# Kernel optimization log

Hardware: AMD Instinct MI355X
Metric: run time of the kernel (lower is better)

The kernel has to match this reference:

```python
import jax, jax.numpy as jnp
import numpy as np

NUM_HEADS = 8
REGION_SIZE = 16
TOPK = 8


def setup_inputs() -> dict:
    key = jax.random.key(0)
    ks = jax.random.split(key, 3)
    B, T, C = 4, 2048, 512
    x = jax.random.normal(ks[0], (B, T, C), dtype=jnp.float32)
    # nn.Linear weights stored as (in, out) so y = x @ W + b
    Wqkv = jax.random.normal(ks[1], (C, 3 * C), dtype=jnp.float32) * 0.02
    bqkv = jnp.zeros((3 * C,), dtype=jnp.float32)
    Wout = jax.random.normal(ks[2], (C, C), dtype=jnp.float32) * 0.02
    bout = jnp.zeros((C,), dtype=jnp.float32)
    return {"x": x, "Wqkv": Wqkv, "bqkv": bqkv, "Wout": Wout, "bout": bout}


def reference(x, Wqkv, bqkv, Wout, bout):
    B, T, C = x.shape
    H, R, K = NUM_HEADS, REGION_SIZE, TOPK
    Dh = C // H
    Nr = T // R  # T chosen divisible by R, so no padding branch
    scale = 1.0 / (Dh ** 0.5)

    qkv = x @ Wqkv + bqkv                                  # (B,T,3C)
    qkv = qkv.reshape(B, T, 3, H, Dh).transpose(2, 0, 3, 1, 4)  # (3,B,H,T,Dh)
    q = qkv[0].reshape(B, H, Nr, R, Dh)
    k = qkv[1].reshape(B, H, Nr, R, Dh)
    v = qkv[2].reshape(B, H, Nr, R, Dh)

    # region-average scores and top-k region selection
    q_avg = q.mean(axis=3)                                 # (B,H,Nr,Dh)
    k_avg = k.mean(axis=3)
    region_score = jnp.einsum('bhqd,bhkd->bhqk', q_avg, k_avg) * scale
    _, topk_idx = jax.lax.top_k(region_score, K)           # (B,H,Nr,K)

    # gather selected K/V region blocks (no dense expand)
    bi = jnp.arange(B)[:, None, None, None]
    hi = jnp.arange(H)[None, :, None, None]
    k_sel = k[bi, hi, topk_idx]                            # (B,H,Nr,K,R,Dh)
    v_sel = v[bi, hi, topk_idx]                            # (B,H,Nr,K,R,Dh)

    # block-sparse attention: each query attends to its K selected regions
    logits = jnp.einsum('bhnrd,bhnksd->bhnrks', q, k_sel) * scale
    logits = logits.reshape(B, H, Nr, R, K * R)
    attn = jax.nn.softmax(logits, axis=-1)
    out = jnp.einsum('bhnrk,bhnkd->bhnrd', attn, v_sel.reshape(B, H, Nr, K * R, Dh))

    out = out.reshape(B, H, T, Dh).transpose(0, 2, 1, 3).reshape(B, T, C)
    return out @ Wout + bout
```

## Files before the change

kernel.cpp:

```cpp
#include <hip/hip_runtime.h>
#include <hip/hip_bf16.h>
#include <math.h>

typedef __bf16 bf16x8 __attribute__((ext_vector_type(8)));
typedef float f32x4 __attribute__((ext_vector_type(4)));

namespace {
constexpr int B  = 4;
constexpr int T  = 2048;
constexpr int C  = 512;
constexpr int H  = 8;
constexpr int Dh = 64;
constexpr int R  = 16;
constexpr int Nr = 128;
constexpr int K  = 8;
constexpr int BT = B * T;
constexpr int QKV_N = 3 * C;
constexpr int KD = 512;
constexpr float SCALE = 0.125f;
}

static __device__ __forceinline__ unsigned short f2bf(float f) {
  unsigned int u = __float_as_uint(f);
  u += 0x7fffu + ((u >> 16) & 1u);
  return (unsigned short)(u >> 16);
}

static __device__ __forceinline__ unsigned cvt_pk_bf16(float lo, float hi) {
  unsigned r;
  asm("v_cvt_pk_bf16_f32 %0, %1, %2" : "=v"(r) : "v"(lo), "v"(hi));
  return r;
}

static __device__ __forceinline__ void gload16(const unsigned short* g, unsigned short* l) {
  __builtin_amdgcn_global_load_lds(
      (const __attribute__((address_space(1))) unsigned int*)g,
      (__attribute__((address_space(3))) unsigned int*)l, 16, 0, 0);
}

static __device__ __forceinline__ unsigned fkey(float f) {
  unsigned u = __float_as_uint(f);
  return (u & 0x80000000u) ? ~u : (u ^ 0x80000000u);
}

__global__ __launch_bounds__(256) void convert_x_kernel(
    const float4* __restrict__ x, ushort4* __restrict__ xbf) {
  const int i = blockIdx.x * 256 + threadIdx.x;
  const float4 v = x[i];
  ushort4 o;
  o.x = f2bf(v.x); o.y = f2bf(v.y); o.z = f2bf(v.z); o.w = f2bf(v.w);
  xbf[i] = o;
}

__global__ __launch_bounds__(256) void transpose_convert_kernel(
    const float* __restrict__ W, unsigned short* __restrict__ Wt, int Kd, int Nd) {
  __shared__ float tile[32][33];
  const int n0 = blockIdx.x * 32, k0 = blockIdx.y * 32;
  const int tx = threadIdx.x & 31, ty = threadIdx.x >> 5;
#pragma unroll
  for (int i = 0; i < 32; i += 8)
    tile[ty + i][tx] = W[(size_t)(k0 + ty + i) * Nd + (n0 + tx)];
  __syncthreads();
#pragma unroll
  for (int i = 0; i < 32; i += 8)
    Wt[(size_t)(n0 + ty + i) * Kd + (k0 + tx)] = f2bf(tile[tx][ty + i]);
}

__device__ __forceinline__ void mfma_mainloop(
    const unsigned short* __restrict__ A, const unsigned short* __restrict__ Bt,
    int bm, int bn, unsigned short* As, unsigned short* Bs, f32x4 (&acc)[4][4]) {
  const int tid = threadIdx.x;
  const int wave = tid >> 6, lane = tid & 63;
  const int wr = wave >> 1, wc = wave & 1;
  const unsigned short* ga = A  + (size_t)(bm + wave * 16 + (lane >> 2)) * KD + (lane & 3) * 8;
  const unsigned short* gb = Bt + (size_t)(bn + wave * 16 + (lane >> 2)) * KD + (lane & 3) * 8;
  unsigned short* lA = As + wave * 512;
  unsigned short* lB = Bs + wave * 512;
  const int fr = lane & 15, kg = lane >> 4;
  const unsigned short* rA = As + (wr * 64 + fr) * 32 + kg * 8;
  const unsigned short* rB = Bs + (wc * 64 + fr) * 32 + kg * 8;
  for (int k0 = 0; k0 < KD; k0 += 32) {
    gload16(ga + k0,                    lA);
    gload16(ga + (size_t)64 * KD + k0,  lA + 2048);
    gload16(gb + k0,                    lB);
    gload16(gb + (size_t)64 * KD + k0,  lB + 2048);
    __syncthreads();
    bf16x8 a[4], b[4];
#pragma unroll
    for (int m = 0; m < 4; ++m) a[m] = *(const bf16x8*)(rA + m * 512);
#pragma unroll
    for (int n = 0; n < 4; ++n) b[n] = *(const bf16x8*)(rB + n * 512);
#pragma unroll
    for (int m = 0; m < 4; ++m)
#pragma unroll
      for (int n = 0; n < 4; ++n)
        acc[m][n] = __builtin_amdgcn_mfma_f32_16x16x32_bf16(a[m], b[n], acc[m][n], 0, 0, 0);
    __syncthreads();
  }
}

__global__ __launch_bounds__(256) void qkv_gemm_mfma_kernel(
    const unsigned short* __restrict__ xbf, const unsigned short* __restrict__ Wt,
    const float* __restrict__ bias,
    unsigned short* __restrict__ qbf, unsigned short* __restrict__ kbf,
    unsigned short* __restrict__ vt) {
  __shared__ unsigned short As[128 * 32];
  __shared__ unsigned short Bs[128 * 32];
  f32x4 acc[4][4] = {};
  const int id = (blockIdx.x & 7) * 96 + (blockIdx.x >> 3);
  const int bn = (id % 12) * 128, bm = (id / 12) * 128;
  mfma_mainloop(xbf, Wt, bm, bn, As, Bs, acc);
  const int lane = threadIdx.x & 63, wave = threadIdx.x >> 6;
  const int wr = wave >> 1, wc = wave & 1;
  const int scol = bn + wc * 64;
  const int s = scol >> 9, h = (scol >> 6) & 7;
  const int b = bm >> 11, t0b = (bm & (T - 1)) + wr * 64;
  const int bh = b * H + h;
  if (s == 2) {
#pragma unroll
    for (int n = 0; n < 4; ++n) {
      const int d = (n * 16 + (lane & 15));
      const float bv = bias[scol + n * 16 + (lane & 15)];
#pragma unroll
      for (int m = 0; m < 4; ++m) {
        const int t = t0b + m * 16 + (lane >> 4) * 4;
        ushort4 pk;
        pk.x = f2bf(acc[m][n][0] + bv); pk.y = f2bf(acc[m][n][1] + bv);
        pk.z = f2bf(acc[m][n][2] + bv); pk.w = f2bf(acc[m][n][3] + bv);
        *(ushort4*)&vt[((size_t)bh * Dh + d) * T + t] = pk;
      }
    }
  } else {
    unsigned short* dstbase = ((s == 0) ? qbf : kbf) + (size_t)bh * T * Dh;
    const int g = lane >> 4, i = lane & 3, a = (lane >> 2) & 3;
#pragma unroll
    for (int n = 0; n < 4; ++n) {
      const float bv = bias[scol + n * 16 + (lane & 15)];
#pragma unroll
      for (int m = 0; m < 4; ++m) {
        const float v0 = acc[m][n][0] + bv, v1 = acc[m][n][1] + bv;
        const float v2 = acc[m][n][2] + bv, v3 = acc[m][n][3] + bv;
        const unsigned p01 = cvt_pk_bf16(v0, v1);
        const unsigned p23 = cvt_pk_bf16(v2, v3);
        const unsigned u01 = (unsigned)__shfl_xor((int)p01, 1);
        const unsigned u23 = (unsigned)__shfl_xor((int)p23, 1);
        const unsigned A  = (lane & 1) ? ((u01 >> 16) | (p01 & 0xFFFF0000u))
                                       : ((p01 & 0xFFFFu) | (u01 << 16));
        const unsigned Bb = (lane & 1) ? ((u23 >> 16) | (p23 & 0xFFFF0000u))
                                       : ((p23 & 0xFFFFu) | (u23 << 16));
        const unsigned w  = (unsigned)__shfl_xor((int)A, 2);
        const unsigned xw = (unsigned)__shfl_xor((int)Bb, 2);
        uint2 res;
        res.x = (lane & 2) ? xw : A;
        res.y = (lane & 2) ? Bb : w;
        const int t = t0b + m * 16 + 4 * g + i;
        const int d = n * 16 + 4 * a;
        *(uint2*)&dstbase[(size_t)t * Dh + d] = res;
      }
    }
  }
}

__global__ __launch_bounds__(256) void out_gemm_mfma_kernel(
    const unsigned short* __restrict__ Abf, const unsigned short* __restrict__ Wt,
    const float* __restrict__ bias, float* __restrict__ out) {
  __shared__ unsigned short As[128 * 32];
  __shared__ unsigned short Bs[128 * 32];
  f32x4 acc[4][4] = {};
  const int id = (blockIdx.x & 7) * 32 + (blockIdx.x >> 3);
  const int bn = (id & 3) * 128, bm = (id >> 2) * 128;
  mfma_mainloop(Abf, Wt, bm, bn, As, Bs, acc);
  const int lane = threadIdx.x & 63, wave = threadIdx.x >> 6;
  const int wr = wave >> 1, wc = wave & 1;
#pragma unroll
  for (int n = 0; n < 4; ++n) {
    const int col = bn + wc * 64 + n * 16 + (lane & 15);
    const float bv = bias[col];
#pragma unroll
    for (int m = 0; m < 4; ++m) {
      const int row = bm + wr * 64 + m * 16 + (lane >> 4) * 4;
#pragma unroll
      for (int r = 0; r < 4; ++r)
        out[(size_t)(row + r) * C + col] = acc[m][n][r] + bv;
    }
  }
}

__global__ __launch_bounds__(256) void x_avg_kernel(
    const float* __restrict__ x, float* __restrict__ xavg) {
  const int blk = blockIdx.x;
  const int c = threadIdx.x;
  const float* xp = x + (size_t)blk * R * C;
  float s0 = 0.f, s1 = 0.f;
#pragma unroll
  for (int r = 0; r < R; ++r) { s0 += xp[r * C + c]; s1 += xp[r * C + c + 256]; }
  xavg[(size_t)blk * C + c] = s0 * 0.0625f;
  xavg[(size_t)blk * C + c + 256] = s1 * 0.0625f;
}

__global__ __launch_bounds__(512) void qkavg_gemm_kernel(
    const float* __restrict__ Xa, const float* __restrict__ W,
    const float* __restrict__ bias,
    float* __restrict__ qavg, float* __restrict__ kavg) {
  __shared__ float As[32][68];
  __shared__ float Bs[32][68];
  const int tid = threadIdx.x;
  const int bm = blockIdx.y * 64;
  const int bn = blockIdx.x * 64;
  const int tm = (tid >> 5) << 2;
  const int tn = (tid & 31) << 1;
  const int arow = tid >> 3;
  const int acol = (tid & 7) << 2;
  const int brow = tid >> 4;
  const int bcol = (tid & 15) << 2;
  float acc[4][2] = {};
  for (int k0 = 0; k0 < KD; k0 += 32) {
    {
      const float4 a = *(const float4*)&Xa[(size_t)(bm + arow) * KD + (k0 + acol)];
      As[acol + 0][arow] = a.x;
      As[acol + 1][arow] = a.y;
      As[acol + 2][arow] = a.z;
      As[acol + 3][arow] = a.w;
      *(float4*)&Bs[brow][bcol] =
          *(const float4*)&W[(size_t)(k0 + brow) * QKV_N + (bn + bcol)];
    }
    __syncthreads();
#pragma unroll
    for (int kk = 0; kk < 32; ++kk) {
      const float4 av = *(const float4*)&As[kk][tm];
      const float2 bv = *(const float2*)&Bs[kk][tn];
      const float aa[4] = {av.x, av.y, av.z, av.w};
#pragma unroll
      for (int i = 0; i < 4; ++i) {
        acc[i][0] += aa[i] * bv.x;
        acc[i][1] += aa[i] * bv.y;
      }
    }
    __syncthreads();
  }
#pragma unroll
  for (int i = 0; i < 4; ++i) {
    const int m = bm + tm + i;
    const int b = m >> 7, n = m & (Nr - 1);
#pragma unroll
    for (int j = 0; j < 2; ++j) {
      const int col = bn + tn + j;
      const int half = col >> 9, h = (col >> 6) & 7, d = col & 63;
      float* dst = half ? kavg : qavg;
      dst[(((size_t)b * H + h) * Nr + n) * Dh + d] = acc[i][j] + bias[col];
    }
  }
}

__global__ __launch_bounds__(64) void topk_kernel(
    const float* __restrict__ qavg, const float* __restrict__ kavg,
    int* __restrict__ topk) {
  const int blk = blockIdx.x;
  const int bh  = blk >> 7;
  const int lane = threadIdx.x;
  const float qv = qavg[(size_t)blk * Dh + lane];
  const float4* k0p = (const float4*)(kavg + ((size_t)bh * Nr + lane) * Dh);
  const float4* k1p = (const float4*)(kavg + ((size_t)bh * Nr + lane + 64) * Dh);
  float d0 = 0.f, d1 = 0.f;
#pragma unroll
  for (int j = 0; j < 16; ++j) {
    const float4 a = k0p[j];
    const float4 bq = k1p[j];
    const float q0 = __shfl(qv, 4 * j + 0);
    const float q1 = __shfl(qv, 4 * j + 1);
    const float q2 = __shfl(qv, 4 * j + 2);
    const float q3 = __shfl(qv, 4 * j + 3);
    d0 += q0 * a.x;  d0 += q1 * a.y;  d0 += q2 * a.z;  d0 += q3 * a.w;
    d1 += q0 * bq.x; d1 += q1 * bq.y; d1 += q2 * bq.z; d1 += q3 * bq.w;
  }
  float v0 = d0, v1 = d1;
#pragma unroll
  for (int j = 0; j < K; ++j) {
    const unsigned long long c0 =
        ((unsigned long long)fkey(v0) << 32) | (unsigned)(127 - lane);
    const unsigned long long c1 =
        ((unsigned long long)fkey(v1) << 32) | (unsigned)(63 - lane);
    unsigned long long c = (c0 > c1) ? c0 : c1;
#pragma unroll
    for (int off = 1; off < 64; off <<= 1) {
      const unsigned long long o = __shfl_xor(c, off);
      c = (o > c) ? o : c;
    }
    const int idx = 127 - (int)(c & 0xffffffffu);
    if (lane == j) topk[blk * K + j] = idx;
    if (idx == lane) v0 = -INFINITY;
    if (idx == lane + 64) v1 = -INFINITY;
  }
}

__global__ __launch_bounds__(64) void attn_mfma_kernel(
    const unsigned short* __restrict__ qbf, const unsigned short* __restrict__ kbf,
    const unsigned short* __restrict__ vt, const int* __restrict__ topk,
    unsigned short* __restrict__ aoutbf) {
  const int phys = blockIdx.x;
  const int blk = (phys & 7) * 512 + (phys >> 3);
  const int bh = blk >> 7, n = blk & (Nr - 1);
  const int b = bh >> 3, h = bh & 7;
  const int lane = threadIdx.x;
  const int q = lane & 15, kg = lane >> 4;
  const int kg1 = kg & 1, kgh = kg >> 1;

  const int rv = topk[blk * K + (lane & 7)];
  int ridx[8];
#pragma unroll
  for (int j = 0; j < 8; ++j) ridx[j] = __shfl(rv, j);

  const unsigned short* qp = qbf + ((size_t)bh * T + n * R + q) * Dh + kg * 8;
  const bf16x8 qf0 = *(const bf16x8*)(qp);
  const bf16x8 qf1 = *(const bf16x8*)(qp + 32);

  f32x4 s[8];
#pragma unroll
  for (int j = 0; j < 8; ++j) {
    const unsigned short* kp = kbf + ((size_t)bh * T + ridx[j] * R + q) * Dh + kg * 8;
    const bf16x8 kf0 = *(const bf16x8*)(kp);
    const bf16x8 kf1 = *(const bf16x8*)(kp + 32);
    f32x4 acc = {};
    acc = __builtin_amdgcn_mfma_f32_16x16x32_bf16(kf0, qf0, acc, 0, 0, 0);
    acc = __builtin_amdgcn_mfma_f32_16x16x32_bf16(kf1, qf1, acc, 0, 0, 0);
    s[j] = acc;
  }

  float mx = s[0][0];
#pragma unroll
  for (int j = 0; j < 8; ++j)
#pragma unroll
    for (int r = 0; r < 4; ++r) mx = fmaxf(mx, s[j][r]);
  mx = fmaxf(mx, __shfl_xor(mx, 16));
  mx = fmaxf(mx, __shfl_xor(mx, 32));
  float sum = 0.f;
#pragma unroll
  for (int j = 0; j < 8; ++j)
#pragma unroll
    for (int r = 0; r < 4; ++r) {
      const float e = __expf((s[j][r] - mx) * SCALE);
      s[j][r] = e; sum += e;
    }
  sum += __shfl_xor(sum, 16);
  sum += __shfl_xor(sum, 32);

  unsigned pk0[8], pk1[8];
#pragma unroll
  for (int j = 0; j < 8; ++j) {
    pk0[j] = cvt_pk_bf16(s[j][0], s[j][1]);
    pk1[j] = cvt_pk_bf16(s[j][2], s[j][3]);
  }

  const int srcA = kg1 * 32 + q;
  const int srcB = kg1 * 32 + 16 + q;
  f32x4 o[4] = {};
#pragma unroll
  for (int t = 0; t < 4; ++t) {
    const unsigned aa0 = __shfl((int)pk0[2 * t], srcA), aa1 = __shfl((int)pk0[2 * t + 1], srcA);
    const unsigned ab0 = __shfl((int)pk1[2 * t], srcA), ab1 = __shfl((int)pk1[2 * t + 1], srcA);
    const unsigned ba0 = __shfl((int)pk0[2 * t], srcB), ba1 = __shfl((int)pk0[2 * t + 1], srcB);
    const unsigned bb0 = __shfl((int)pk1[2 * t], srcB), bb1 = __shfl((int)pk1[2 * t + 1], srcB);
    union { uint4 u; bf16x8 v; } bu;
    bu.u.x = kgh ? aa1 : aa0;
    bu.u.y = kgh ? ab1 : ab0;
    bu.u.z = kgh ? ba1 : ba0;
    bu.u.w = kgh ? bb1 : bb0;
    const int reg = kgh ? ridx[2 * t + 1] : ridx[2 * t];
    const size_t tok = (size_t)reg * R + kg1 * 8;
#pragma unroll
    for (int dt = 0; dt < 4; ++dt) {
      const bf16x8 af = *(const bf16x8*)(vt + ((size_t)bh * Dh + 16 * dt + q) * T + tok);
      o[dt] = __builtin_amdgcn_mfma_f32_16x16x32_bf16(af, bu.v, o[dt], 0, 0, 0);
    }
  }

  const float inv = 1.0f / sum;
  unsigned short* dst = aoutbf + ((size_t)b * T + n * R + q) * C + h * Dh;
#pragma unroll
  for (int dt = 0; dt < 4; ++dt) {
    const unsigned plo = cvt_pk_bf16(o[dt][0] * inv, o[dt][1] * inv);
    const unsigned phi = cvt_pk_bf16(o[dt][2] * inv, o[dt][3] * inv);
    uint2 st; st.x = plo; st.y = phi;
    *(uint2*)(dst + 16 * dt + kg * 4) = st;
  }
}

extern "C" void kernel_launch(void* const* d_in, const int* in_sizes, int n_in,
                              void* d_out, int out_size, void* d_ws, size_t ws_size,
                              hipStream_t stream) {
  const float* x    = (const float*)d_in[0];
  const float* Wqkv = (const float*)d_in[1];
  const float* bqkv = (const float*)d_in[2];
  const float* Wout = (const float*)d_in[3];
  const float* bout = (const float*)d_in[4];
  float* out = (float*)d_out;

  float* ws = (float*)d_ws;
  const size_t bhtd = (size_t)B * H * T * Dh;
  const size_t navg = (size_t)B * H * Nr * Dh;
  float* qavg = ws;
  float* kavg = qavg + navg;
  float* xavg = kavg + navg;
  unsigned short* qbf    = (unsigned short*)(xavg + navg);
  unsigned short* kbf    = qbf + bhtd;
  unsigned short* vt     = kbf + bhtd;
  unsigned short* xbf    = vt + bhtd;
  unsigned short* wqkvt  = xbf + bhtd;
  unsigned short* woutt  = wqkvt + (size_t)QKV_N * KD;
  unsigned short* aoutbf = woutt + (size_t)C * KD;
  int* topk = (int*)(aoutbf + bhtd);

  convert_x_kernel<<<4096, 256, 0, stream>>>((const float4*)x, (ushort4*)xbf);
  transpose_convert_kernel<<<dim3(QKV_N / 32, KD / 32), 256, 0, stream>>>(Wqkv, wqkvt, KD, QKV_N);
  transpose_convert_kernel<<<dim3(C / 32, KD / 32), 256, 0, stream>>>(Wout, woutt, KD, C);
  x_avg_kernel<<<B * Nr, 256, 0, stream>>>(x, xavg);
  qkavg_gemm_kernel<<<dim3(1024 / 64, (B * Nr) / 64), 512, 0, stream>>>(xavg, Wqkv, bqkv, qavg, kavg);
  topk_kernel<<<B * H * Nr, 64, 0, stream>>>(qavg, kavg, topk);
  qkv_gemm_mfma_kernel<<<QKV_N / 128 * (BT / 128), 256, 0, stream>>>(xbf, wqkvt, bqkv, qbf, kbf, vt);
  attn_mfma_kernel<<<B * H * Nr, 64, 0, stream>>>(qbf, kbf, vt, topk, aoutbf);
  out_gemm_mfma_kernel<<<C / 128 * (BT / 128), 256, 0, stream>>>(aoutbf, woutt, bout, out);
}
```

Measured before the change: 132.4 us.

## Fuse output projection into attention kernel and merge prep kernels

Attention now runs one 512-thread block per (batch, region) with one wave per head. Each block writes its 16x512 bf16 attention output to padded LDS, then multiplies by the transposed Wout with MFMA to produce the final fp32 output directly. This removes the aout round trip through global memory and one launch. The x conversion and region averaging are merged into one kernel, and the two weight transposes into another. The trade-off is that each block re-reads all of Wout from global or L2 with no LDS reuse, and the grid shrinks from 4096 to 512 blocks.

```diff
diff --git a/kernel.cpp b/kernel.cpp
--- a/kernel.cpp
+++ b/kernel.cpp
@@ -17,6 +17,7 @@
 constexpr int BT = B * T;
 constexpr int QKV_N = 3 * C;
 constexpr int KD = 512;
+constexpr int ATT_LD = 520;
 constexpr float SCALE = 0.125f;
 }
 
@@ -43,19 +44,35 @@
   return (u & 0x80000000u) ? ~u : (u ^ 0x80000000u);
 }
 
-__global__ __launch_bounds__(256) void convert_x_kernel(
-    const float4* __restrict__ x, ushort4* __restrict__ xbf) {
-  const int i = blockIdx.x * 256 + threadIdx.x;
-  const float4 v = x[i];
-  ushort4 o;
-  o.x = f2bf(v.x); o.y = f2bf(v.y); o.z = f2bf(v.z); o.w = f2bf(v.w);
-  xbf[i] = o;
-}
-
-__global__ __launch_bounds__(256) void transpose_convert_kernel(
-    const float* __restrict__ W, unsigned short* __restrict__ Wt, int Kd, int Nd) {
+__global__ __launch_bounds__(128) void prep_x_kernel(
+    const float* __restrict__ x, unsigned short* __restrict__ xbf,
+    float* __restrict__ xavg) {
+  const int blk = blockIdx.x;
+  const int c4 = threadIdx.x;
+  const float4* xp = (const float4*)(x + (size_t)blk * R * C) + c4;
+  ushort4* xb = (ushort4*)(xbf + (size_t)blk * R * C) + c4;
+  float sx = 0.f, sy = 0.f, sz = 0.f, sw = 0.f;
+#pragma unroll
+  for (int r = 0; r < R; ++r) {
+    const float4 v = xp[(size_t)r * 128];
+    ushort4 o;
+    o.x = f2bf(v.x); o.y = f2bf(v.y); o.z = f2bf(v.z); o.w = f2bf(v.w);
+    xb[(size_t)r * 128] = o;
+    sx += v.x; sy += v.y; sz += v.z; sw += v.w;
+  }
+  float4 av; av.x = sx * 0.0625f; av.y = sy * 0.0625f;
+  av.z = sz * 0.0625f; av.w = sw * 0.0625f;
+  *((float4*)(xavg + (size_t)blk * C) + c4) = av;
+}
+
+__global__ __launch_bounds__(256) void wt_transpose_kernel(
+    const float* __restrict__ Wqkv, const float* __restrict__ Wout,
+    unsigned short* __restrict__ wqkvt, unsigned short* __restrict__ woutt) {
   __shared__ float tile[32][33];
-  const int n0 = blockIdx.x * 32, k0 = blockIdx.y * 32;
+  int id = blockIdx.x;
+  const float* W; unsigned short* Wt; int Nd, n0, k0;
+  if (id < 768) { W = Wqkv; Wt = wqkvt; Nd = QKV_N; n0 = (id % 48) * 32; k0 = (id / 48) * 32; }
+  else { id -= 768; W = Wout; Wt = woutt; Nd = C; n0 = (id % 16) * 32; k0 = (id / 16) * 32; }
   const int tx = threadIdx.x & 31, ty = threadIdx.x >> 5;
 #pragma unroll
   for (int i = 0; i < 32; i += 8)
@@ -63,7 +80,7 @@
   __syncthreads();
 #pragma unroll
   for (int i = 0; i < 32; i += 8)
-    Wt[(size_t)(n0 + ty + i) * Kd + (k0 + tx)] = f2bf(tile[tx][ty + i]);
+    Wt[(size_t)(n0 + ty + i) * KD + (k0 + tx)] = f2bf(tile[tx][ty + i]);
 }
 
 __device__ __forceinline__ void mfma_mainloop(
@@ -159,43 +176,6 @@
       }
     }
   }
-}
-
-__global__ __launch_bounds__(256) void out_gemm_mfma_kernel(
-    const unsigned short* __restrict__ Abf, const unsigned short* __restrict__ Wt,
-    const float* __restrict__ bias, float* __restrict__ out) {
-  __shared__ unsigned short As[128 * 32];
-  __shared__ unsigned short Bs[128 * 32];
-  f32x4 acc[4][4] = {};
-  const int id = (blockIdx.x & 7) * 32 + (blockIdx.x >> 3);
-  const int bn = (id & 3) * 128, bm = (id >> 2) * 128;
-  mfma_mainloop(Abf, Wt, bm, bn, As, Bs, acc);
-  const int lane = threadIdx.x & 63, wave = threadIdx.x >> 6;
-  const int wr = wave >> 1, wc = wave & 1;
-#pragma unroll
-  for (int n = 0; n < 4; ++n) {
-    const int col = bn + wc * 64 + n * 16 + (lane & 15);
-    const float bv = bias[col];
-#pragma unroll
-    for (int m = 0; m < 4; ++m) {
-      const int row = bm + wr * 64 + m * 16 + (lane >> 4) * 4;
-#pragma unroll
-      for (int r = 0; r < 4; ++r)
-        out[(size_t)(row + r) * C + col] = acc[m][n][r] + bv;
-    }
-  }
-}
-
-__global__ __launch_bounds__(256) void x_avg_kernel(
-    const float* __restrict__ x, float* __restrict__ xavg) {
-  const int blk = blockIdx.x;
-  const int c = threadIdx.x;
-  const float* xp = x + (size_t)blk * R * C;
-  float s0 = 0.f, s1 = 0.f;
-#pragma unroll
-  for (int r = 0; r < R; ++r) { s0 += xp[r * C + c]; s1 += xp[r * C + c + 256]; }
-  xavg[(size_t)blk * C + c] = s0 * 0.0625f;
-  xavg[(size_t)blk * C + c + 256] = s1 * 0.0625f;
 }
 
 __global__ __launch_bounds__(512) void qkavg_gemm_kernel(
@@ -293,22 +273,26 @@
   }
 }
 
-__global__ __launch_bounds__(64) void attn_mfma_kernel(
+__global__ __launch_bounds__(512) void attn_fused_kernel(
     const unsigned short* __restrict__ qbf, const unsigned short* __restrict__ kbf,
     const unsigned short* __restrict__ vt, const int* __restrict__ topk,
-    unsigned short* __restrict__ aoutbf) {
+    const unsigned short* __restrict__ woutt, const float* __restrict__ bout,
+    float* __restrict__ out) {
+  __shared__ unsigned short att[16 * ATT_LD];
   const int phys = blockIdx.x;
-  const int blk = (phys & 7) * 512 + (phys >> 3);
-  const int bh = blk >> 7, n = blk & (Nr - 1);
-  const int b = bh >> 3, h = bh & 7;
-  const int lane = threadIdx.x;
+  const int blk = (phys & 7) * 64 + (phys >> 3);
+  const int b = blk >> 7, n = blk & (Nr - 1);
+  const int tid = threadIdx.x;
+  const int h = tid >> 6, lane = tid & 63;
+  const int bh = b * H + h;
+  const int sblk = bh * Nr + n;
   const int q = lane & 15, kg = lane >> 4;
   const int kg1 = kg & 1, kgh = kg >> 1;
 
-  const int rv = topk[blk * K + (lane & 7)];
+  const int rvx = topk[sblk * K + (lane & 7)];
   int ridx[8];
 #pragma unroll
-  for (int j = 0; j < 8; ++j) ridx[j] = __shfl(rv, j);
+  for (int j = 0; j < 8; ++j) ridx[j] = __shfl(rvx, j);
 
   const unsigned short* qp = qbf + ((size_t)bh * T + n * R + q) * Dh + kg * 8;
   const bf16x8 qf0 = *(const bf16x8*)(qp);
@@ -375,13 +359,33 @@
   }
 
   const float inv = 1.0f / sum;
-  unsigned short* dst = aoutbf + ((size_t)b * T + n * R + q) * C + h * Dh;
+  unsigned short* arow = att + q * ATT_LD + h * 64;
 #pragma unroll
   for (int dt = 0; dt < 4; ++dt) {
-    const unsigned plo = cvt_pk_bf16(o[dt][0] * inv, o[dt][1] * inv);
-    const unsigned phi = cvt_pk_bf16(o[dt][2] * inv, o[dt][3] * inv);
-    uint2 st; st.x = plo; st.y = phi;
-    *(uint2*)(dst + 16 * dt + kg * 4) = st;
+    uint2 st;
+    st.x = cvt_pk_bf16(o[dt][0] * inv, o[dt][1] * inv);
+    st.y = cvt_pk_bf16(o[dt][2] * inv, o[dt][3] * inv);
+    *(uint2*)(arow + 16 * dt + kg * 4) = st;
+  }
+  __syncthreads();
+
+  f32x4 oacc[4] = {};
+  for (int t = 0; t < 16; ++t) {
+    const bf16x8 af = *(const bf16x8*)(att + q * ATT_LD + t * 32 + kg * 8);
+#pragma unroll
+    for (int nt = 0; nt < 4; ++nt) {
+      const bf16x8 bf = *(const bf16x8*)(woutt + (size_t)(h * 64 + nt * 16 + q) * KD + t * 32 + kg * 8);
+      oacc[nt] = __builtin_amdgcn_mfma_f32_16x16x32_bf16(af, bf, oacc[nt], 0, 0, 0);
+    }
+  }
+  const int row0 = b * T + n * R + (lane >> 4) * 4;
+#pragma unroll
+  for (int nt = 0; nt < 4; ++nt) {
+    const int col = h * 64 + nt * 16 + q;
+    const float bb = bout[col];
+#pragma unroll
+    for (int r = 0; r < 4; ++r)
+      out[(size_t)(row0 + r) * C + col] = oacc[nt][r] + bb;
   }
 }
 
@@ -407,16 +411,12 @@
   unsigned short* xbf    = vt + bhtd;
   unsigned short* wqkvt  = xbf + bhtd;
   unsigned short* woutt  = wqkvt + (size_t)QKV_N * KD;
-  unsigned short* aoutbf = woutt + (size_t)C * KD;
-  int* topk = (int*)(aoutbf + bhtd);
-
-  convert_x_kernel<<<4096, 256, 0, stream>>>((const float4*)x, (ushort4*)xbf);
-  transpose_convert_kernel<<<dim3(QKV_N / 32, KD / 32), 256, 0, stream>>>(Wqkv, wqkvt, KD, QKV_N);
-  transpose_convert_kernel<<<dim3(C / 32, KD / 32), 256, 0, stream>>>(Wout, woutt, KD, C);
-  x_avg_kernel<<<B * Nr, 256, 0, stream>>>(x, xavg);
+  int* topk = (int*)(woutt + (size_t)C * KD);
+
+  prep_x_kernel<<<B * Nr, 128, 0, stream>>>(x, xbf, xavg);
+  wt_transpose_kernel<<<768 + 256, 256, 0, stream>>>(Wqkv, Wout, wqkvt, woutt);
   qkavg_gemm_kernel<<<dim3(1024 / 64, (B * Nr) / 64), 512, 0, stream>>>(xavg, Wqkv, bqkv, qavg, kavg);
   topk_kernel<<<B * H * Nr, 64, 0, stream>>>(qavg, kavg, topk);
   qkv_gemm_mfma_kernel<<<QKV_N / 128 * (BT / 128), 256, 0, stream>>>(xbf, wqkvt, bqkv, qbf, kbf, vt);
-  attn_mfma_kernel<<<B * H * Nr, 64, 0, stream>>>(qbf, kbf, vt, topk, aoutbf);
-  out_gemm_mfma_kernel<<<C / 128 * (BT / 128), 256, 0, stream>>>(aoutbf, woutt, bout, out);
-}
+  attn_fused_kernel<<<B * Nr, 512, 0, stream>>>(qbf, kbf, vt, topk, woutt, bout, out);
+}
```

New measurement: 141.6 us. 1.07x slower.

## Merge prep kernels and run region-average GEMM alongside QKV GEMM

Applied to the files above, without the earlier changes.

Replaces five preprocessing launches with one combined kernel. The x conversion to bf16 and the per-region mean are computed in a single pass over x, and the two weight transposes are handled by blocks of the same launch. The fp32 region-average GEMM is folded into the QKV MFMA GEMM launch as extra blocks, so both run concurrently. This cuts launch count and one full read of x, at the cost of heterogeneous blocks sharing one launch and a smaller shared tile layout for the averaging GEMM.

```diff
diff --git a/kernel.cpp b/kernel.cpp
--- a/kernel.cpp
+++ b/kernel.cpp
@@ -43,19 +43,35 @@
   return (u & 0x80000000u) ? ~u : (u ^ 0x80000000u);
 }
 
-__global__ __launch_bounds__(256) void convert_x_kernel(
-    const float4* __restrict__ x, ushort4* __restrict__ xbf) {
-  const int i = blockIdx.x * 256 + threadIdx.x;
-  const float4 v = x[i];
-  ushort4 o;
-  o.x = f2bf(v.x); o.y = f2bf(v.y); o.z = f2bf(v.z); o.w = f2bf(v.w);
-  xbf[i] = o;
-}
-
-__global__ __launch_bounds__(256) void transpose_convert_kernel(
-    const float* __restrict__ W, unsigned short* __restrict__ Wt, int Kd, int Nd) {
+__global__ __launch_bounds__(256) void prep_combo_kernel(
+    const float* __restrict__ x, const float* __restrict__ Wqkv,
+    const float* __restrict__ Wout,
+    unsigned short* __restrict__ xbf, float* __restrict__ xavg,
+    unsigned short* __restrict__ wqkvt, unsigned short* __restrict__ woutt) {
+  int id = blockIdx.x;
+  if (id >= 1024) {
+    const int rid = (id - 1024) * 2 + (threadIdx.x >> 7);
+    const int c4 = threadIdx.x & 127;
+    const float4* xp = (const float4*)(x + (size_t)rid * R * C) + c4;
+    ushort4* xb = (ushort4*)(xbf + (size_t)rid * R * C) + c4;
+    float sx = 0.f, sy = 0.f, sz = 0.f, sw = 0.f;
+#pragma unroll
+    for (int r = 0; r < R; ++r) {
+      const float4 v = xp[(size_t)r * 128];
+      ushort4 o;
+      o.x = f2bf(v.x); o.y = f2bf(v.y); o.z = f2bf(v.z); o.w = f2bf(v.w);
+      xb[(size_t)r * 128] = o;
+      sx += v.x; sy += v.y; sz += v.z; sw += v.w;
+    }
+    float4 av; av.x = sx * 0.0625f; av.y = sy * 0.0625f;
+    av.z = sz * 0.0625f; av.w = sw * 0.0625f;
+    *((float4*)(xavg + (size_t)rid * C) + c4) = av;
+    return;
+  }
   __shared__ float tile[32][33];
-  const int n0 = blockIdx.x * 32, k0 = blockIdx.y * 32;
+  const float* W; unsigned short* Wt; int Nd, n0, k0;
+  if (id < 768) { W = Wqkv; Wt = wqkvt; Nd = QKV_N; n0 = (id % 48) * 32; k0 = (id / 48) * 32; }
+  else { id -= 768; W = Wout; Wt = woutt; Nd = C; n0 = (id % 16) * 32; k0 = (id / 16) * 32; }
   const int tx = threadIdx.x & 31, ty = threadIdx.x >> 5;
 #pragma unroll
   for (int i = 0; i < 32; i += 8)
@@ -63,7 +79,7 @@
   __syncthreads();
 #pragma unroll
   for (int i = 0; i < 32; i += 8)
-    Wt[(size_t)(n0 + ty + i) * Kd + (k0 + tx)] = f2bf(tile[tx][ty + i]);
+    Wt[(size_t)(n0 + ty + i) * KD + (k0 + tx)] = f2bf(tile[tx][ty + i]);
 }
 
 __device__ __forceinline__ void mfma_mainloop(
@@ -99,155 +115,119 @@
   }
 }
 
-__global__ __launch_bounds__(256) void qkv_gemm_mfma_kernel(
+__global__ __launch_bounds__(256) void mega_gemm_kernel(
     const unsigned short* __restrict__ xbf, const unsigned short* __restrict__ Wt,
-    const float* __restrict__ bias,
+    const float* __restrict__ bqkv,
     unsigned short* __restrict__ qbf, unsigned short* __restrict__ kbf,
-    unsigned short* __restrict__ vt) {
-  __shared__ unsigned short As[128 * 32];
-  __shared__ unsigned short Bs[128 * 32];
-  f32x4 acc[4][4] = {};
-  const int id = (blockIdx.x & 7) * 96 + (blockIdx.x >> 3);
-  const int bn = (id % 12) * 128, bm = (id / 12) * 128;
-  mfma_mainloop(xbf, Wt, bm, bn, As, Bs, acc);
-  const int lane = threadIdx.x & 63, wave = threadIdx.x >> 6;
-  const int wr = wave >> 1, wc = wave & 1;
-  const int scol = bn + wc * 64;
-  const int s = scol >> 9, h = (scol >> 6) & 7;
-  const int b = bm >> 11, t0b = (bm & (T - 1)) + wr * 64;
-  const int bh = b * H + h;
-  if (s == 2) {
-#pragma unroll
-    for (int n = 0; n < 4; ++n) {
-      const int d = (n * 16 + (lane & 15));
-      const float bv = bias[scol + n * 16 + (lane & 15)];
-#pragma unroll
-      for (int m = 0; m < 4; ++m) {
-        const int t = t0b + m * 16 + (lane >> 4) * 4;
-        ushort4 pk;
-        pk.x = f2bf(acc[m][n][0] + bv); pk.y = f2bf(acc[m][n][1] + bv);
-        pk.z = f2bf(acc[m][n][2] + bv); pk.w = f2bf(acc[m][n][3] + bv);
-        *(ushort4*)&vt[((size_t)bh * Dh + d) * T + t] = pk;
+    unsigned short* __restrict__ vt,
+    const float* __restrict__ xavg, const float* __restrict__ Wqkv,
+    float* __restrict__ qavg, float* __restrict__ kavg) {
+  __shared__ unsigned short SMEM[2 * 128 * 32];
+  const int gid = blockIdx.x;
+  const int tid = threadIdx.x;
+  if (gid < 768) {
+    unsigned short* As = SMEM;
+    unsigned short* Bs = SMEM + 128 * 32;
+    f32x4 acc[4][4] = {};
+    const int id = (gid & 7) * 96 + (gid >> 3);
+    const int bn = (id % 12) * 128, bm = (id / 12) * 128;
+    mfma_mainloop(xbf, Wt, bm, bn, As, Bs, acc);
+    const int lane = tid & 63, wave = tid >> 6;
+    const int wr = wave >> 1, wc = wave & 1;
+    const int scol = bn + wc * 64;
+    const int s = scol >> 9, h = (scol >> 6) & 7;
+    const int b = bm >> 11, t0b = (bm & (T - 1)) + wr * 64;
+    const int bh = b * H + h;
+    if (s == 2) {
+#pragma unroll
+      for (int n = 0; n < 4; ++n) {
+        const int d = (n * 16 + (lane & 15));
+        const float bv = bqkv[scol + n * 16 + (lane & 15)];
+#pragma unroll
+        for (int m = 0; m < 4; ++m) {
+          const int t = t0b + m * 16 + (lane >> 4) * 4;
+          ushort4 pk;
+          pk.x = f2bf(acc[m][n][0] + bv); pk.y = f2bf(acc[m][n][1] + bv);
+          pk.z = f2bf(acc[m][n][2] + bv); pk.w = f2bf(acc[m][n][3] + bv);
+          *(ushort4*)&vt[((size_t)bh * Dh + d) * T + t] = pk;
+        }
       }
+    } else {
+      unsigned short* dstbase = ((s == 0) ? qbf : kbf) + (size_t)bh * T * Dh;
+      const int g = lane >> 4, i = lane & 3, a = (lane >> 2) & 3;
+#pragma unroll
+      for (int n = 0; n < 4; ++n) {
+        const float bv = bqkv[scol + n * 16 + (lane & 15)];
+#pragma unroll
+        for (int m = 0; m < 4; ++m) {
+          const float v0 = acc[m][n][0] + bv, v1 = acc[m][n][1] + bv;
+          const float v2 = acc[m][n][2] + bv, v3 = acc[m][n][3] + bv;
+          const unsigned p01 = cvt_pk_bf16(v0, v1);
+          const unsigned p23 = cvt_pk_bf16(v2, v3);
+          const unsigned u01 = (unsigned)__shfl_xor((int)p01, 1);
+          const unsigned u23 = (unsigned)__shfl_xor((int)p23, 1);
+          const unsigned A  = (lane & 1) ? ((u01 >> 16) | (p01 & 0xFFFF0000u))
+                                         : ((p01 & 0xFFFFu) | (u01 << 16));
+          const unsigned Bb = (lane & 1) ? ((u23 >> 16) | (p23 & 0xFFFF0000u))
+                                         : ((p23 & 0xFFFFu) | (u23 << 16));
+          const unsigned w  = (unsigned)__shfl_xor((int)A, 2);
+          const unsigned xw = (unsigned)__shfl_xor((int)Bb, 2);
+          uint2 res;
+          res.x = (lane & 2) ? xw : A;
+          res.y = (lane & 2) ? Bb : w;
+          const int t = t0b + m * 16 + 4 * g + i;
+          const int d = n * 16 + 4 * a;
+          *(uint2*)&dstbase[(size_t)t * Dh + d] = res;
+        }
+      }
     }
   } else {
-    unsigned short* dstbase = ((s == 0) ? qbf : kbf) + (size_t)bh * T * Dh;
-    const int g = lane >> 4, i = lane & 3, a = (lane >> 2) & 3;
-#pragma unroll
-    for (int n = 0; n < 4; ++n) {
-      const float bv = bias[scol + n * 16 + (lane & 15)];
-#pragma unroll
-      for (int m = 0; m < 4; ++m) {
-        const float v0 = acc[m][n][0] + bv, v1 = acc[m][n][1] + bv;
-        const float v2 = acc[m][n][2] + bv, v3 = acc[m][n][3] + bv;
-        const unsigned p01 = cvt_pk_bf16(v0, v1);
-        const unsigned p23 = cvt_pk_bf16(v2, v3);
-        const unsigned u01 = (unsigned)__shfl_xor((int)p01, 1);
-        const unsigned u23 = (unsigned)__shfl_xor((int)p23, 1);
-        const unsigned A  = (lane & 1) ? ((u01 >> 16) | (p01 & 0xFFFF0000u))
-                                       : ((p01 & 0xFFFFu) | (u01 << 16));
-        const unsigned Bb = (lane & 1) ? ((u23 >> 16) | (p23 & 0xFFFF0000u))
-                                       : ((p23 & 0xFFFFu) | (u23 << 16));
-        const unsigned w  = (unsigned)__shfl_xor((int)A, 2);
-        const unsigned xw = (unsigned)__shfl_xor((int)Bb, 2);
-        uint2 res;
-        res.x = (lane & 2) ? xw : A;
-        res.y = (lane & 2) ? Bb : w;
-        const int t = t0b + m * 16 + 4 * g + i;
-        const int d = n * 16 + 4 * a;
-        *(uint2*)&dstbase[(size_t)t * Dh + d] = res;
+    float* Asf = (float*)SMEM;
+    float* Bsf = (float*)SMEM + 32 * 36;
+    const int id2 = gid - 768;
+    const int bm = (id2 >> 4) * 32, bn = (id2 & 15) * 64;
+    const int arow = tid >> 3;
+    const int acol = (tid & 7) << 2;
+    const int brow = tid >> 4;
+    const int bcol = (tid & 15) << 2;
+    const int tm = (tid >> 5) << 2;
+    const int tn = (tid & 31) << 1;
+    float acc[4][2] = {};
+    for (int k0 = 0; k0 < KD; k0 += 32) {
+      const float4 a = *(const float4*)&xavg[(size_t)(bm + arow) * KD + (k0 + acol)];
+      Asf[(acol + 0) * 36 + arow] = a.x;
+      Asf[(acol + 1) * 36 + arow] = a.y;
+      Asf[(acol + 2) * 36 + arow] = a.z;
+      Asf[(acol + 3) * 36 + arow] = a.w;
+#pragma unroll
+      for (int p = 0; p < 2; ++p)
+        *(float4*)&Bsf[(brow + 16 * p) * 68 + bcol] =
+            *(const float4*)&Wqkv[(size_t)(k0 + brow + 16 * p) * QKV_N + (bn + bcol)];
+      __syncthreads();
+#pragma unroll
+      for (int kk = 0; kk < 32; ++kk) {
+        const float4 av = *(const float4*)&Asf[kk * 36 + tm];
+        const float2 bv = *(const float2*)&Bsf[kk * 68 + tn];
+        const float aa[4] = {av.x, av.y, av.z, av.w};
+#pragma unroll
+        for (int i = 0; i < 4; ++i) {
+          acc[i][0] += aa[i] * bv.x;
+          acc[i][1] += aa[i] * bv.y;
+        }
       }
-    }
-  }
-}
-
-__global__ __launch_bounds__(256) void out_gemm_mfma_kernel(
-    const unsigned short* __restrict__ Abf, const unsigned short* __restrict__ Wt,
-    const float* __restrict__ bias, float* __restrict__ out) {
-  __shared__ unsigned short As[128 * 32];
-  __shared__ unsigned short Bs[128 * 32];
-  f32x4 acc[4][4] = {};
-  const int id = (blockIdx.x & 7) * 32 + (blockIdx.x >> 3);
-  const int bn = (id & 3) * 128, bm = (id >> 2) * 128;
-  mfma_mainloop(Abf, Wt, bm, bn, As, Bs, acc);
-  const int lane = threadIdx.x & 63, wave = threadIdx.x >> 6;
-  const int wr = wave >> 1, wc = wave & 1;
-#pragma unroll
-  for (int n = 0; n < 4; ++n) {
-    const int col = bn + wc * 64 + n * 16 + (lane & 15);
-    const float bv = bias[col];
-#pragma unroll
-    for (int m = 0; m < 4; ++m) {
-      const int row = bm + wr * 64 + m * 16 + (lane >> 4) * 4;
-#pragma unroll
-      for (int r = 0; r < 4; ++r)
-        out[(size_t)(row + r) * C + col] = acc[m][n][r] + bv;
-    }
-  }
-}
-
-__global__ __launch_bounds__(256) void x_avg_kernel(
-    const float* __restrict__ x, float* __restrict__ xavg) {
-  const int blk = blockIdx.x;
-  const int c = threadIdx.x;
-  const float* xp = x + (size_t)blk * R * C;
-  float s0 = 0.f, s1 = 0.f;
-#pragma unroll
-  for (int r = 0; r < R; ++r) { s0 += xp[r * C + c]; s1 += xp[r * C + c + 256]; }
-  xavg[(size_t)blk * C + c] = s0 * 0.0625f;
-  xavg[(size_t)blk * C + c + 256] = s1 * 0.0625f;
-}
-
-__global__ __launch_bounds__(512) void qkavg_gemm_kernel(
-    const float* __restrict__ Xa, const float* __restrict__ W,
-    const float* __restrict__ bias,
-    float* __restrict__ qavg, float* __restrict__ kavg) {
-  __shared__ float As[32][68];
-  __shared__ float Bs[32][68];
-  const int tid = threadIdx.x;
-  const int bm = blockIdx.y * 64;
-  const int bn = blockIdx.x * 64;
-  const int tm = (tid >> 5) << 2;
-  const int tn = (tid & 31) << 1;
-  const int arow = tid >> 3;
-  const int acol = (tid & 7) << 2;
-  const int brow = tid >> 4;
-  const int bcol = (tid & 15) << 2;
-  float acc[4][2] = {};
-  for (int k0 = 0; k0 < KD; k0 += 32) {
-    {
-      const float4 a = *(const float4*)&Xa[(size_t)(bm + arow) * KD + (k0 + acol)];
-      As[acol + 0][arow] = a.x;
-      As[acol + 1][arow] = a.y;
-      As[acol + 2][arow] = a.z;
-      As[acol + 3][arow] = a.w;
-      *(float4*)&Bs[brow][bcol] =
-          *(const float4*)&W[(size_t)(k0 + brow) * QKV_N + (bn + bcol)];
-    }
-    __syncthreads();
-#pragma unroll
-    for (int kk = 0; kk < 32; ++kk) {
-      const float4 av = *(const float4*)&As[kk][tm];
-      const float2 bv = *(const float2*)&Bs[kk][tn];
-      const float aa[4] = {av.x, av.y, av.z, av.w};
-#pragma unroll
-      for (int i = 0; i < 4; ++i) {
-        acc[i][0] += aa[i] * bv.x;
-        acc[i][1] += aa[i] * bv.y;
+      __syncthreads();
+    }
+#pragma unroll
+    for (int i = 0; i < 4; ++i) {
+      const int m = bm + tm + i;
+      const int b = m >> 7, n = m & (Nr - 1);
+#pragma unroll
+      for (int j = 0; j < 2; ++j) {
+        const int col = bn + tn + j;
+        const int half = col >> 9, h = (col >> 6) & 7, d = col & 63;
+        float* dst = half ? kavg : qavg;
+        dst[(((size_t)b * H + h) * Nr + n) * Dh + d] = acc[i][j] + bqkv[col];
       }
-    }
-    __syncthreads();
-  }
-#pragma unroll
-  for (int i = 0; i < 4; ++i) {
-    const int m = bm + tm + i;
-    const int b = m >> 7, n = m & (Nr - 1);
-#pragma unroll
-    for (int j = 0; j < 2; ++j) {
-      const int col = bn + tn + j;
-      const int half = col >> 9, h = (col >> 6) & 7, d = col & 63;
-      float* dst = half ? kavg : qavg;
-      dst[(((size_t)b * H + h) * Nr + n) * Dh + d] = acc[i][j] + bias[col];
     }
   }
 }
@@ -382,6 +362,31 @@
     const unsigned phi = cvt_pk_bf16(o[dt][2] * inv, o[dt][3] * inv);
     uint2 st; st.x = plo; st.y = phi;
     *(uint2*)(dst + 16 * dt + kg * 4) = st;
+  }
+}
+
+__global__ __launch_bounds__(256) void out_gemm_mfma_kernel(
+    const unsigned short* __restrict__ Abf, const unsigned short* __restrict__ Wt,
+    const float* __restrict__ bias, float* __restrict__ out) {
+  __shared__ unsigned short As[128 * 32];
+  __shared__ unsigned short Bs[128 * 32];
+  f32x4 acc[4][4] = {};
+  const int id = (blockIdx.x & 7) * 32 + (blockIdx.x >> 3);
+  const int bn = (id & 3) * 128, bm = (id >> 2) * 128;
+  mfma_mainloop(Abf, Wt, bm, bn, As, Bs, acc);
+  const int lane = threadIdx.x & 63, wave = threadIdx.x >> 6;
+  const int wr = wave >> 1, wc = wave & 1;
+#pragma unroll
+  for (int n = 0; n < 4; ++n) {
+    const int col = bn + wc * 64 + n * 16 + (lane & 15);
+    const float bv = bias[col];
+#pragma unroll
+    for (int m = 0; m < 4; ++m) {
+      const int row = bm + wr * 64 + m * 16 + (lane >> 4) * 4;
+#pragma unroll
+      for (int r = 0; r < 4; ++r)
+        out[(size_t)(row + r) * C + col] = acc[m][n][r] + bv;
+    }
   }
 }
 
@@ -410,13 +415,10 @@
   unsigned short* aoutbf = woutt + (size_t)C * KD;
   int* topk = (int*)(aoutbf + bhtd);
 
-  convert_x_kernel<<<4096, 256, 0, stream>>>((const float4*)x, (ushort4*)xbf);
-  transpose_convert_kernel<<<dim3(QKV_N / 32, KD / 32), 256, 0, stream>>>(Wqkv, wqkvt, KD, QKV_N);
-  transpose_convert_kernel<<<dim3(C / 32, KD / 32), 256, 0, stream>>>(Wout, woutt, KD, C);
-  x_avg_kernel<<<B * Nr, 256, 0, stream>>>(x, xavg);
-  qkavg_gemm_kernel<<<dim3(1024 / 64, (B * Nr) / 64), 512, 0, stream>>>(xavg, Wqkv, bqkv, qavg, kavg);
+  prep_combo_kernel<<<1280, 256, 0, stream>>>(x, Wqkv, Wout, xbf, xavg, wqkvt, woutt);
+  mega_gemm_kernel<<<1024, 256, 0, stream>>>(xbf, wqkvt, bqkv, qbf, kbf, vt,
+                                             xavg, Wqkv, qavg, kavg);
   topk_kernel<<<B * H * Nr, 64, 0, stream>>>(qavg, kavg, topk);
-  qkv_gemm_mfma_kernel<<<QKV_N / 128 * (BT / 128), 256, 0, stream>>>(xbf, wqkvt, bqkv, qbf, kbf, vt);
   attn_mfma_kernel<<<B * H * Nr, 64, 0, stream>>>(qbf, kbf, vt, topk, aoutbf);
   out_gemm_mfma_kernel<<<C / 128 * (BT / 128), 256, 0, stream>>>(aoutbf, woutt, bout, out);
 }
```

Result: faster. 126.7 us (-4.4%).
